# Kernel optimization log

Measured on AMD Instinct MI355X. Metric: run time of the kernel, lower is better.

Reference implementation:

```python
import jax, jax.numpy as jnp
import numpy as np

N_NODES = 50000
N_EDGES = 800000
IN_CH = 128
HID_CH = 128
OUT_CH = 10
NUM_GRAPHS = 128


def setup_inputs() -> dict:
    key = jax.random.key(0)
    ks = jax.random.split(key, 10)
    x = jax.random.normal(ks[0], (N_NODES, IN_CH), dtype=jnp.float32)
    edge_index = jax.random.randint(ks[1], (2, N_EDGES), 0, N_NODES, dtype=jnp.int64)
    batch = jnp.sort(jax.random.randint(ks[2], (N_NODES,), 0, NUM_GRAPHS, dtype=jnp.int64))
    s1 = 1.0 / np.sqrt(IN_CH)
    s2 = 1.0 / np.sqrt(HID_CH)
    W1 = jax.random.uniform(ks[3], (IN_CH, HID_CH), jnp.float32, -s1, s1)
    b1 = jnp.zeros((HID_CH,), jnp.float32)
    W2 = jax.random.uniform(ks[4], (HID_CH, HID_CH), jnp.float32, -s2, s2)
    b2 = jnp.zeros((HID_CH,), jnp.float32)
    Wc = jax.random.uniform(ks[5], (HID_CH, OUT_CH), jnp.float32, -s2, s2)
    bc = jax.random.uniform(ks[6], (OUT_CH,), jnp.float32, -s2, s2)
    return {"x": x, "edge_index": edge_index, "batch": batch,
            "W1": W1, "b1": b1, "W2": W2, "b2": b2, "Wc": Wc, "bc": bc}


def _gcn_norm(edge_index, num_nodes):
    # add self-loops, compute symmetric normalization deg^-1/2[src]*deg^-1/2[dst]
    loop = jnp.arange(num_nodes, dtype=edge_index.dtype)
    src = jnp.concatenate([edge_index[0], loop])
    dst = jnp.concatenate([edge_index[1], loop])
    deg = jax.ops.segment_sum(jnp.ones_like(dst, dtype=jnp.float32), dst,
                              num_segments=num_nodes)
    dinv = jnp.where(deg > 0, jax.lax.rsqrt(deg), 0.0)
    norm = dinv[src] * dinv[dst]
    return src, dst, norm


def _gcn_conv(h, src, dst, norm, W, b, num_nodes):
    h = h @ W                                    # [N, out]
    msg = h[src] * norm[:, None]                 # [E+N, out] gather + scale
    agg = jax.ops.segment_sum(msg, dst, num_segments=num_nodes)
    return agg + b


def reference(x, edge_index, batch, W1, b1, W2, b2, Wc, bc):
    n = x.shape[0]
    src, dst, norm = _gcn_norm(edge_index, n)
    h = jax.nn.relu(_gcn_conv(x, src, dst, norm, W1, b1, n))
    h = jax.nn.relu(_gcn_conv(h, src, dst, norm, W2, b2, n))
    # global mean pool over graphs
    sums = jax.ops.segment_sum(h, batch, num_segments=NUM_GRAPHS)
    cnts = jax.ops.segment_sum(jnp.ones((n,), jnp.float32), batch,
                               num_segments=NUM_GRAPHS)
    pooled = sums / jnp.maximum(cnts, 1.0)[:, None]
    # dropout is identity in eval mode
    return pooled @ Wc + bc
```

## Files before the change

### kernel.cpp

```cpp
#include <hip/hip_runtime.h>

#define N_NODES 50000
#define N_EDGES 800000
#define CH 128
#define NOUT 10
#define NUM_GRAPHS 128
#define GR 64
#define GEMM_BLOCKS ((N_NODES + GR - 1) / GR)
#define FILL_SEGS 200
#define FILL_CHUNK (N_EDGES / FILL_SEGS)
#define DST_RANGE (N_NODES / 8)
#define DEG_CAP 64

typedef __attribute__((ext_vector_type(8))) short bf16x8;
typedef __attribute__((ext_vector_type(4))) float f32x4;

union FragU { uint4 u; bf16x8 s; };

__device__ __forceinline__ unsigned pack_bf16(float a, float b) {
    unsigned ua = __float_as_uint(a), ub = __float_as_uint(b);
    ua += 0x7fffu + ((ua >> 16) & 1u);
    ub += 0x7fffu + ((ub >> 16) & 1u);
    return (ua >> 16) | (ub & 0xffff0000u);
}

__device__ __forceinline__ unsigned short cvt_bf16(float v) {
    unsigned u = __float_as_uint(v);
    u += 0x7fffu + ((u >> 16) & 1u);
    return (unsigned short)(u >> 16);
}

__global__ __launch_bounds__(256) void k_prep(const float* __restrict__ W1,
                                              const float* __restrict__ W2,
                                              unsigned short* __restrict__ Wb1,
                                              unsigned short* __restrict__ Wb2,
                                              int* __restrict__ fill_pos,
                                              float* __restrict__ psum) {
    if (blockIdx.x < 2) {
        const float* W = blockIdx.x ? W2 : W1;
        unsigned short* Wb = blockIdx.x ? Wb2 : Wb1;
        for (int i = threadIdx.x; i < CH * CH; i += 256) {
            int k = i >> 7, n = i & 127;
            Wb[((((k >> 3) << 7) + n) << 3) + (k & 7)] = cvt_bf16(W[i]);
        }
    } else if (blockIdx.x < 198) {
        int idx = (blockIdx.x - 2) * 256 + threadIdx.x;
        if (idx < N_NODES) fill_pos[idx] = 0;
    } else {
        psum[(blockIdx.x - 198) * 256 + threadIdx.x] = 0.f;
    }
}

template <bool SCALE>
__device__ __forceinline__ void gemm_body9(const float* __restrict__ X,
                                           const unsigned short* __restrict__ Wb,
                                           unsigned short* __restrict__ Yb,
                                           const int* __restrict__ cnt,
                                           int bid) {
    const int tid = threadIdx.x;
    const int w = tid >> 6;
    const int lane = tid & 63;
    const int m = lane & 15;
    const int quad = lane >> 4;
    const int row0 = bid * GR + w * 16;

    int row_a = row0 + m;
    if (row_a > N_NODES - 1) row_a = N_NODES - 1;
    const float4* Xr = (const float4*)(X + (size_t)row_a * CH) + quad * 2;

    float4 a[8];
    #pragma unroll
    for (int ks = 0; ks < 4; ++ks) {
        a[ks * 2]     = Xr[ks * 8];
        a[ks * 2 + 1] = Xr[ks * 8 + 1];
    }

    f32x4 acc[8];
    #pragma unroll
    for (int ct = 0; ct < 8; ++ct) acc[ct] = (f32x4){0.f, 0.f, 0.f, 0.f};

    const uint4* Wq = (const uint4*)Wb;
    #pragma unroll
    for (int ks = 0; ks < 4; ++ks) {
        FragU af;
        af.u.x = pack_bf16(a[ks * 2].x, a[ks * 2].y);
        af.u.y = pack_bf16(a[ks * 2].z, a[ks * 2].w);
        af.u.z = pack_bf16(a[ks * 2 + 1].x, a[ks * 2 + 1].y);
        af.u.w = pack_bf16(a[ks * 2 + 1].z, a[ks * 2 + 1].w);
        const int kg = ks * 4 + quad;
        #pragma unroll
        for (int ct = 0; ct < 8; ++ct) {
            FragU bfu;
            bfu.u = Wq[kg * 128 + ct * 16 + m];
            acc[ct] = __builtin_amdgcn_mfma_f32_16x16x32_bf16(af.s, bfu.s, acc[ct], 0, 0, 0);
        }
    }

    #pragma unroll
    for (int r = 0; r < 4; ++r) {
        int row = row0 + quad * 4 + r;
        if (row < N_NODES) {
            float dv = SCALE ? rsqrtf((float)(cnt[row] + 1)) : 1.0f;
            unsigned short* yrow = Yb + (size_t)row * CH + m;
            #pragma unroll
            for (int ct = 0; ct < 8; ++ct)
                yrow[ct * 16] = cvt_bf16(SCALE ? acc[ct][r] * dv : acc[ct][r]);
        }
    }
}

__global__ __launch_bounds__(256) void k_gemm_fill(const float* __restrict__ X,
                                                   const unsigned short* __restrict__ Wb,
                                                   unsigned short* __restrict__ Yb,
                                                   const int* __restrict__ src,
                                                   const int* __restrict__ dst,
                                                   int* __restrict__ fill_pos,
                                                   int* __restrict__ csr_src) {
    if (blockIdx.x < GEMM_BLOCKS) {
        gemm_body9<false>(X, Wb, Yb, nullptr, blockIdx.x);
    } else {
        const int b = blockIdx.x - GEMM_BLOCKS;
        const int rng = b & 7;
        const int seg = b >> 3;
        const int lo = rng * DST_RANGE, hi = lo + DST_RANGE;
        const int base = seg * FILL_CHUNK;
        for (int it = threadIdx.x * 4; it < FILL_CHUNK; it += 1024) {
            int e = base + it;
            int4 d4 = *(const int4*)(dst + e);
            #pragma unroll
            for (int k = 0; k < 4; ++k) {
                int d = (&d4.x)[k];
                if (d >= lo && d < hi) {
                    int slot = atomicAdd(&fill_pos[d], 1);
                    if (slot < DEG_CAP) csr_src[(d << 6) + slot] = src[e + k];
                }
            }
        }
    }
}

__global__ __launch_bounds__(256) void k_gemm9b(const float* __restrict__ X,
                                                const unsigned short* __restrict__ Wb,
                                                unsigned short* __restrict__ Yb,
                                                const int* __restrict__ cnt) {
    gemm_body9<true>(X, Wb, Yb, cnt, blockIdx.x);
}

template <bool HAS_W, bool POOL>
__device__ __forceinline__ void gather_body(const unsigned* __restrict__ tb,
                                            const int* __restrict__ csr_src,
                                            const int* __restrict__ cnt,
                                            const float* __restrict__ bias,
                                            float* __restrict__ h,
                                            const int* __restrict__ batch,
                                            float* __restrict__ psum) {
    const int wid = threadIdx.x >> 6;
    const int lane = threadIdx.x & 63;
    const int sub = lane >> 4;
    const int cidx = lane & 15;
    const int v = blockIdx.x * 4 + wid;

    int lenc = cnt[v];
    const float dv = rsqrtf((float)(lenc + 1));
    int len = lenc > DEG_CAP ? DEG_CAP : lenc;

    int u_l = 0;
    float w_l = 0.f;
    if (lane < len) {
        u_l = csr_src[(v << 6) + lane];
        if (HAS_W) w_l = rsqrtf((float)(cnt[u_l] + 1));
    }

    const uint4* tbq = (const uint4*)tb;
    float x[8];
    #pragma unroll
    for (int t = 0; t < 8; ++t) x[t] = 0.f;

    int j = 0;
    for (; j + 8 <= len; j += 8) {
        int i0 = j + sub, i1 = j + 4 + sub;
        int ua = __shfl(u_l, i0);
        int ub = __shfl(u_l, i1);
        float wa = HAS_W ? __shfl(w_l, i0) : 1.f;
        float wb = HAS_W ? __shfl(w_l, i1) : 1.f;
        uint4 qa = tbq[(size_t)ua * 16 + cidx];
        uint4 qb = tbq[(size_t)ub * 16 + cidx];
        #pragma unroll
        for (int t = 0; t < 4; ++t) {
            unsigned ra = ((const unsigned*)&qa)[t];
            x[2 * t]     = fmaf(wa, __uint_as_float(ra << 16), x[2 * t]);
            x[2 * t + 1] = fmaf(wa, __uint_as_float(ra & 0xffff0000u), x[2 * t + 1]);
        }
        #pragma unroll
        for (int t = 0; t < 4; ++t) {
            unsigned rb = ((const unsigned*)&qb)[t];
            x[2 * t]     = fmaf(wb, __uint_as_float(rb << 16), x[2 * t]);
            x[2 * t + 1] = fmaf(wb, __uint_as_float(rb & 0xffff0000u), x[2 * t + 1]);
        }
    }
    for (; j < len; j += 4) {
        int idx = j + sub;
        bool act = idx < len;
        int idx_c = act ? idx : 0;
        int u = __shfl(u_l, idx_c);
        float w;
        if (HAS_W) { float ws = __shfl(w_l, idx_c); w = act ? ws : 0.f; }
        else       { w = act ? 1.f : 0.f; }
        uint4 q = tbq[(size_t)u * 16 + cidx];
        #pragma unroll
        for (int t = 0; t < 4; ++t) {
            unsigned r = ((const unsigned*)&q)[t];
            x[2 * t]     = fmaf(w, __uint_as_float(r << 16), x[2 * t]);
            x[2 * t + 1] = fmaf(w, __uint_as_float(r & 0xffff0000u), x[2 * t + 1]);
        }
    }
    {
        uint4 q = tbq[(size_t)v * 16 + cidx];
        float w = (sub == 0) ? (HAS_W ? dv : 1.f) : 0.f;
        #pragma unroll
        for (int t = 0; t < 4; ++t) {
            unsigned r = ((const unsigned*)&q)[t];
            x[2 * t]     = fmaf(w, __uint_as_float(r << 16), x[2 * t]);
            x[2 * t + 1] = fmaf(w, __uint_as_float(r & 0xffff0000u), x[2 * t + 1]);
        }
    }

    #pragma unroll
    for (int t = 0; t < 8; ++t) {
        x[t] += __shfl_xor(x[t], 16);
        x[t] += __shfl_xor(x[t], 32);
    }

    const float4* b4 = (const float4*)bias;
    float4 b0 = b4[cidx * 2], b1 = b4[cidx * 2 + 1];
    float4 o0, o1;
    o0.x = fmaxf(fmaf(dv, x[0], b0.x), 0.f);
    o0.y = fmaxf(fmaf(dv, x[1], b0.y), 0.f);
    o0.z = fmaxf(fmaf(dv, x[2], b0.z), 0.f);
    o0.w = fmaxf(fmaf(dv, x[3], b0.w), 0.f);
    o1.x = fmaxf(fmaf(dv, x[4], b1.x), 0.f);
    o1.y = fmaxf(fmaf(dv, x[5], b1.y), 0.f);
    o1.z = fmaxf(fmaf(dv, x[6], b1.z), 0.f);
    o1.w = fmaxf(fmaf(dv, x[7], b1.w), 0.f);

    if (POOL) {
        __shared__ float sh[4][128];
        __shared__ int sg[4];
        if (lane == 0) sg[wid] = batch[v];
        if (sub == 0) {
            *(float4*)&sh[wid][cidx * 8]     = o0;
            *(float4*)&sh[wid][cidx * 8 + 4] = o1;
        }
        __syncthreads();
        const int tid = threadIdx.x;
        if (tid < 128) {
            int g0 = sg[0], g1 = sg[1], g2 = sg[2], g3 = sg[3];
            float v0 = sh[0][tid], v1 = sh[1][tid], v2 = sh[2][tid], v3 = sh[3][tid];
            if (g0 == g3) {
                atomicAdd(&psum[g0 * CH + tid], v0 + v1 + v2 + v3);
            } else {
                if (g0 == g1) v1 += v0; else atomicAdd(&psum[g0 * CH + tid], v0);
                if (g1 == g2) v2 += v1; else atomicAdd(&psum[g1 * CH + tid], v1);
                if (g2 == g3) v3 += v2; else atomicAdd(&psum[g2 * CH + tid], v2);
                atomicAdd(&psum[g3 * CH + tid], v3);
            }
        }
    } else {
        if (sub == 0) {
            float4* hq = (float4*)(h + (size_t)v * CH);
            hq[cidx * 2]     = o0;
            hq[cidx * 2 + 1] = o1;
        }
    }
}

__global__ __launch_bounds__(256) void k_gather_hw(const unsigned* __restrict__ tb,
                                                   const int* __restrict__ csr_src,
                                                   const int* __restrict__ cnt,
                                                   const float* __restrict__ b,
                                                   float* __restrict__ h) {
    gather_body<true, false>(tb, csr_src, cnt, b, h, nullptr, nullptr);
}

__global__ __launch_bounds__(256) void k_gather_pool(const unsigned* __restrict__ tb,
                                                     const int* __restrict__ csr_src,
                                                     const int* __restrict__ cnt,
                                                     const float* __restrict__ b,
                                                     const int* __restrict__ batch,
                                                     float* __restrict__ psum) {
    gather_body<false, true>(tb, csr_src, cnt, b, nullptr, batch, psum);
}

__global__ __launch_bounds__(128) void k_classify(const float* __restrict__ psum,
                                                  const int* __restrict__ batch,
                                                  const float* __restrict__ Wc,
                                                  const float* __restrict__ bc,
                                                  float* __restrict__ out) {
    __shared__ float p[CH];
    __shared__ float sinv;
    int g = blockIdx.x;
    int tid = threadIdx.x;
    if (tid == 0) {
        int lo = 0, hi = N_NODES;
        while (lo < hi) { int mid = (lo + hi) >> 1; if (batch[mid] < g) lo = mid + 1; else hi = mid; }
        int start = lo;
        lo = 0; hi = N_NODES;
        while (lo < hi) { int mid = (lo + hi) >> 1; if (batch[mid] < g + 1) lo = mid + 1; else hi = mid; }
        sinv = 1.0f / fmaxf((float)(lo - start), 1.0f);
    }
    __syncthreads();
    p[tid] = psum[g * CH + tid] * sinv;
    __syncthreads();
    if (tid < NOUT) {
        float acc = bc[tid];
        #pragma unroll 4
        for (int k = 0; k < CH; ++k) acc += p[k] * Wc[k * NOUT + tid];
        out[g * NOUT + tid] = acc;
    }
}

extern "C" void kernel_launch(void* const* d_in, const int* in_sizes, int n_in,
                              void* d_out, int out_size, void* d_ws, size_t ws_size,
                              hipStream_t stream) {
    const float* x     = (const float*)d_in[0];
    const int*   ei    = (const int*)d_in[1];
    const int*   batch = (const int*)d_in[2];
    const float* W1    = (const float*)d_in[3];
    const float* b1    = (const float*)d_in[4];
    const float* W2    = (const float*)d_in[5];
    const float* b2    = (const float*)d_in[6];
    const float* Wc    = (const float*)d_in[7];
    const float* bc    = (const float*)d_in[8];
    float* out = (float*)d_out;

    const int* src = ei;
    const int* dst = ei + N_EDGES;

    int*            fill_pos = (int*)d_ws;
    int*            csr_src  = fill_pos + N_NODES;
    unsigned short* wb1      = (unsigned short*)(csr_src + (size_t)N_NODES * DEG_CAP);
    unsigned short* wb2      = wb1 + CH * CH;
    unsigned short* tb       = wb2 + CH * CH;
    float*          hbuf     = (float*)(tb + (size_t)N_NODES * CH);
    float*          psum     = hbuf + (size_t)N_NODES * CH;

    k_prep<<<198 + 64, 256, 0, stream>>>(W1, W2, wb1, wb2, fill_pos, psum);

    k_gemm_fill<<<GEMM_BLOCKS + FILL_SEGS * 8, 256, 0, stream>>>(
        x, wb1, tb, src, dst, fill_pos, csr_src);

    k_gather_hw<<<N_NODES / 4, 256, 0, stream>>>((unsigned*)tb, csr_src, fill_pos, b1, hbuf);

    k_gemm9b<<<GEMM_BLOCKS, 256, 0, stream>>>(hbuf, wb2, tb, fill_pos);

    k_gather_pool<<<N_NODES / 4, 256, 0, stream>>>((unsigned*)tb, csr_src, fill_pos, b2,
                                                   batch, psum);

    k_classify<<<NUM_GRAPHS, 128, 0, stream>>>(psum, batch, Wc, bc, out);
}
```

Before: 246.5 us.

## Build CSR with per-range LDS counters instead of global atomics

```diff
diff --git a/kernel.cpp b/kernel.cpp
--- a/kernel.cpp
+++ b/kernel.cpp
@@ -7,9 +7,8 @@
 #define NUM_GRAPHS 128
 #define GR 64
 #define GEMM_BLOCKS ((N_NODES + GR - 1) / GR)
-#define FILL_SEGS 200
-#define FILL_CHUNK (N_EDGES / FILL_SEGS)
-#define DST_RANGE (N_NODES / 8)
+#define FILL_RANGES 128
+#define RANGE_N ((N_NODES + FILL_RANGES - 1) / FILL_RANGES)
 #define DEG_CAP 64
 
 typedef __attribute__((ext_vector_type(8))) short bf16x8;
@@ -34,7 +33,6 @@
                                               const float* __restrict__ W2,
                                               unsigned short* __restrict__ Wb1,
                                               unsigned short* __restrict__ Wb2,
-                                              int* __restrict__ fill_pos,
                                               float* __restrict__ psum) {
     if (blockIdx.x < 2) {
         const float* W = blockIdx.x ? W2 : W1;
@@ -43,11 +41,8 @@
             int k = i >> 7, n = i & 127;
             Wb[((((k >> 3) << 7) + n) << 3) + (k & 7)] = cvt_bf16(W[i]);
         }
-    } else if (blockIdx.x < 198) {
-        int idx = (blockIdx.x - 2) * 256 + threadIdx.x;
-        if (idx < N_NODES) fill_pos[idx] = 0;
     } else {
-        psum[(blockIdx.x - 198) * 256 + threadIdx.x] = 0.f;
+        psum[(blockIdx.x - 2) * 256 + threadIdx.x] = 0.f;
     }
 }
 
@@ -119,23 +114,25 @@
     if (blockIdx.x < GEMM_BLOCKS) {
         gemm_body9<false>(X, Wb, Yb, nullptr, blockIdx.x);
     } else {
-        const int b = blockIdx.x - GEMM_BLOCKS;
-        const int rng = b & 7;
-        const int seg = b >> 3;
-        const int lo = rng * DST_RANGE, hi = lo + DST_RANGE;
-        const int base = seg * FILL_CHUNK;
-        for (int it = threadIdx.x * 4; it < FILL_CHUNK; it += 1024) {
-            int e = base + it;
+        __shared__ int lcnt[RANGE_N];
+        const int rng = blockIdx.x - GEMM_BLOCKS;
+        const int lo = rng * RANGE_N;
+        const int hi = (lo + RANGE_N < N_NODES) ? lo + RANGE_N : N_NODES;
+        for (int i = threadIdx.x; i < RANGE_N; i += 256) lcnt[i] = 0;
+        __syncthreads();
+        for (int e = threadIdx.x * 4; e < N_EDGES; e += 1024) {
             int4 d4 = *(const int4*)(dst + e);
             #pragma unroll
             for (int k = 0; k < 4; ++k) {
                 int d = (&d4.x)[k];
                 if (d >= lo && d < hi) {
-                    int slot = atomicAdd(&fill_pos[d], 1);
+                    int slot = atomicAdd(&lcnt[d - lo], 1);
                     if (slot < DEG_CAP) csr_src[(d << 6) + slot] = src[e + k];
                 }
             }
         }
+        __syncthreads();
+        for (int i = threadIdx.x; lo + i < hi; i += 256) fill_pos[lo + i] = lcnt[i];
     }
 }
 
@@ -344,9 +341,9 @@
     float*          hbuf     = (float*)(tb + (size_t)N_NODES * CH);
     float*          psum     = hbuf + (size_t)N_NODES * CH;
 
-    k_prep<<<198 + 64, 256, 0, stream>>>(W1, W2, wb1, wb2, fill_pos, psum);
-
-    k_gemm_fill<<<GEMM_BLOCKS + FILL_SEGS * 8, 256, 0, stream>>>(
+    k_prep<<<2 + 64, 256, 0, stream>>>(W1, W2, wb1, wb2, psum);
+
+    k_gemm_fill<<<GEMM_BLOCKS + FILL_RANGES, 256, 0, stream>>>(
         x, wb1, tb, src, dst, fill_pos, csr_src);
 
     k_gather_hw<<<N_NODES / 4, 256, 0, stream>>>((unsigned*)tb, csr_src, fill_pos, b1, hbuf);
```

Result: slower. 657.9 us (+166.9%).
